# Performance work log

Measured on AMD Instinct MI355X. Metric: run time of the kernel, lower is better.

The kernel has to match this reference:

```python
import jax, jax.numpy as jnp
import numpy as np

VOCAB = 100000
EMB = 256
HID = 512
HH = HID // 2  # per-direction hidden
NTAGS = 12
START = 10
STOP = 11
SEQ = 2048
NEG = -10000.0


def setup_inputs() -> dict:
    key = jax.random.key(0)
    ks = jax.random.split(key, 18)
    s = 0.05
    inp = {
        "sentence": jax.random.randint(ks[0], (SEQ,), 0, VOCAB, dtype=jnp.int64 if jax.config.jax_enable_x64 else jnp.int32),
        "tags": jax.random.randint(ks[1], (SEQ,), 0, 10, dtype=jnp.int64 if jax.config.jax_enable_x64 else jnp.int32),
        "embed": jax.random.normal(ks[2], (VOCAB, EMB), jnp.float32) * s,
        "Wih_f": jax.random.normal(ks[3], (4 * HH, EMB), jnp.float32) * s,
        "Whh_f": jax.random.normal(ks[4], (4 * HH, HH), jnp.float32) * s,
        "bih_f": jax.random.normal(ks[5], (4 * HH,), jnp.float32) * s,
        "bhh_f": jax.random.normal(ks[6], (4 * HH,), jnp.float32) * s,
        "Wih_b": jax.random.normal(ks[7], (4 * HH, EMB), jnp.float32) * s,
        "Whh_b": jax.random.normal(ks[8], (4 * HH, HH), jnp.float32) * s,
        "bih_b": jax.random.normal(ks[9], (4 * HH,), jnp.float32) * s,
        "bhh_b": jax.random.normal(ks[10], (4 * HH,), jnp.float32) * s,
        "W_out": jax.random.normal(ks[11], (NTAGS, HID), jnp.float32) * s,
        "b_out": jax.random.normal(ks[12], (NTAGS,), jnp.float32) * s,
        "h0": jax.random.normal(ks[14], (2, HH), jnp.float32),
        "c0": jax.random.normal(ks[15], (2, HH), jnp.float32),
    }
    trans = jax.random.normal(ks[13], (NTAGS, NTAGS), jnp.float32)
    trans = trans.at[START, :].set(NEG)  # never transition INTO start
    trans = trans.at[:, STOP].set(NEG)   # never transition FROM stop
    inp["transitions"] = trans
    return inp


def _lstm_dir(x, h0, c0, Wih, Whh, bih, bhh):
    # x: [T, E]; PyTorch gate order i, f, g, o
    pre = x @ Wih.T + bih + bhh  # [T, 4*HH] precomputed input projection
    def step(carry, p):
        h, c = carry
        g = p + Whh @ h
        i, f, gg, o = jnp.split(g, 4)
        i = jax.nn.sigmoid(i)
        f = jax.nn.sigmoid(f)
        gg = jnp.tanh(gg)
        o = jax.nn.sigmoid(o)
        c = f * c + i * gg
        h = o * jnp.tanh(c)
        return (h, c), h
    _, hs = jax.lax.scan(step, (h0, c0), pre)
    return hs  # [T, HH]


def _forward_impl(sentence, tags, embed, Wih_f, Whh_f, bih_f, bhh_f,
                  Wih_b, Whh_b, bih_b, bhh_b, W_out, b_out, transitions, h0, c0):
    x = embed[sentence]  # [T, E]
    hf = _lstm_dir(x, h0[0], c0[0], Wih_f, Whh_f, bih_f, bhh_f)
    hb = jnp.flip(_lstm_dir(jnp.flip(x, 0), h0[1], c0[1], Wih_b, Whh_b, bih_b, bhh_b), 0)
    feats = jnp.concatenate([hf, hb], axis=-1) @ W_out.T + b_out  # [T, NTAGS]

    # CRF forward algorithm: log-semiring scan over time
    fv0 = jnp.full((NTAGS,), NEG, feats.dtype).at[START].set(0.0)
    def crf_step(fv, emit):
        # transitions[next, prev]; logsumexp over prev
        fv = jax.nn.logsumexp(fv[None, :] + transitions + emit[:, None], axis=1)
        return fv, None
    fv, _ = jax.lax.scan(crf_step, fv0, feats)
    forward_score = jax.nn.logsumexp(fv + transitions[STOP])

    # gold path score
    prev = jnp.concatenate([jnp.array([START], dtype=tags.dtype), tags[:-1]])
    emit_gold = jnp.take_along_axis(feats, tags[:, None], axis=1)[:, 0]
    gold_score = jnp.sum(transitions[tags, prev]) + jnp.sum(emit_gold) + transitions[STOP, tags[-1]]

    return forward_score - gold_score


def reference(sentence, tags, embed, Wih_f, Whh_f, bih_f, bhh_f,
              Wih_b, Whh_b, bih_b, bhh_b, W_out, b_out, transitions, h0, c0):
    return _forward_impl(sentence, tags, embed, Wih_f, Whh_f, bih_f, bhh_f,
                         Wih_b, Whh_b, bih_b, bhh_b, W_out, b_out, transitions, h0, c0)
```

## Files before the change

kernel.cpp:

```cpp
#include <hip/hip_runtime.h>
#include <hip/hip_bf16.h>
#include <stdint.h>

#define SEQ   2048
#define EMB   256
#define HHD   256
#define GATES 1024
#define NTAGS 12
#define START 10
#define STOP  11
#define CCH   16
#define CLEN  128

__device__ __forceinline__ int sdot4(uint32_t a, uint32_t b, int c) {
#if __has_builtin(__builtin_amdgcn_sdot4)
  return __builtin_amdgcn_sdot4((int)a, (int)b, c, false);
#else
  int r = c;
#pragma unroll
  for (int i = 0; i < 4; i++) {
    int av = (int)(signed char)((a >> (8 * i)) & 255);
    int bv = (int)(signed char)((b >> (8 * i)) & 255);
    r += av * bv;
  }
  return r;
#endif
}

__device__ __forceinline__ float fsig(float x) {
  float e = __expf(-x);
  return __builtin_amdgcn_rcpf(1.0f + e);
}

__global__ __launch_bounds__(256) void k_quant(const float* __restrict__ whh_f,
                                               const float* __restrict__ whh_b,
                                               uint32_t* __restrict__ q4,
                                               float* __restrict__ scales) {
  const int row  = (blockIdx.x * 256 + threadIdx.x) >> 6;
  const int lane = threadIdx.x & 63;
  const int d = row >> 10, r = row & 1023;
  const float4 w = *(const float4*)((d ? whh_b : whh_f) + (long)r * HHD + lane * 4);
  float m = fmaxf(fmaxf(fabsf(w.x), fabsf(w.y)), fmaxf(fabsf(w.z), fabsf(w.w)));
#pragma unroll
  for (int off = 32; off; off >>= 1) m = fmaxf(m, __shfl_xor(m, off, 64));
  m = fmaxf(m, 1e-20f);
  const float inv = 127.f / m;
  int a = (int)rintf(w.x * inv), b = (int)rintf(w.y * inv);
  int c = (int)rintf(w.z * inv), e = (int)rintf(w.w * inv);
  q4[row * 64 + lane] = (uint32_t)(a & 255) | ((uint32_t)(b & 255) << 8) |
                        ((uint32_t)(c & 255) << 16) | ((uint32_t)(e & 255) << 24);
  if (lane == 0) scales[row] = m / 127.f;
}

__global__ __launch_bounds__(256) void k_proj(const int* __restrict__ sentence,
                                              const float* __restrict__ embed,
                                              const float* __restrict__ Wih_f,
                                              const float* __restrict__ bih_f,
                                              const float* __restrict__ bhh_f,
                                              const float* __restrict__ Wih_b,
                                              const float* __restrict__ bih_b,
                                              const float* __restrict__ bhh_b,
                                              float* __restrict__ pre) {
  const int dir = blockIdx.y;
  const int t0  = blockIdx.x * 8;
  const float* Wih = dir ? Wih_b : Wih_f;
  const float* bih = dir ? bih_b : bih_f;
  const float* bhh = dir ? bhh_b : bhh_f;

  __shared__ float xs[8][256];
  const int tid = threadIdx.x;
#pragma unroll
  for (int i = 0; i < 8; i++) {
    int s = sentence[t0 + i];
    xs[i][tid] = embed[(long)s * EMB + tid];
  }
  __syncthreads();

  const int r0 = tid * 4;
  float acc[4][8];
#pragma unroll
  for (int j = 0; j < 4; j++)
#pragma unroll
    for (int t = 0; t < 8; t++) acc[j][t] = 0.f;

  const float4* W4 = (const float4*)Wih;
  for (int kq = 0; kq < 64; kq++) {
    float4 w[4];
#pragma unroll
    for (int j = 0; j < 4; j++) w[j] = W4[(r0 + j) * 64 + kq];
#pragma unroll
    for (int t = 0; t < 8; t++) {
      float4 xv = ((const float4*)xs[t])[kq];
#pragma unroll
      for (int j = 0; j < 4; j++)
        acc[j][t] += w[j].x * xv.x + w[j].y * xv.y + w[j].z * xv.z + w[j].w * xv.w;
    }
  }
#pragma unroll
  for (int j = 0; j < 4; j++) {
    float bsum = bih[r0 + j] + bhh[r0 + j];
#pragma unroll
    for (int t = 0; t < 8; t++)
      pre[((long)(dir * SEQ + t0 + t)) * GATES + r0 + j] = acc[j][t] + bsum;
  }
}

__global__ __launch_bounds__(512, 1) void k_lstm(const uint32_t* __restrict__ q4,
                                                 const float* __restrict__ scales,
                                                 const float* __restrict__ pre,
                                                 const float* __restrict__ h0,
                                                 const float* __restrict__ c0,
                                                 float* __restrict__ hs) {
  const int dir = blockIdx.x;
  const int L   = threadIdx.x;
  const int u   = L >> 1;
  const int odd = L & 1;

  __shared__ __align__(16) uint8_t hbuf[2][256];

  const int rA = (odd ? 512 : 0) + u;
  const int rB = rA + 256;
  const long base = (long)dir * GATES;

  const uint4* qq = (const uint4*)q4;
  uint4 wA[16], wB[16];
#pragma unroll
  for (int j = 0; j < 16; j++) wA[j] = qq[(base + rA) * 16 + j];
#pragma unroll
  for (int j = 0; j < 16; j++) wB[j] = qq[(base + rB) * 16 + j];
  const float sA = scales[base + rA];
  const float sB = scales[base + rB];

  if (L < 256) {
    float v = h0[dir * HHD + L] * (127.f / 4.f);
    v = fminf(fmaxf(v, -127.f), 127.f);
    hbuf[0][L] = (uint8_t)(int)rintf(v);
  }
  float c_st = c0[dir * HHD + u];
  __syncthreads();

  const float* pd = pre + (long)dir * SEQ * GATES;
  float* hsd      = hs  + (long)dir * SEQ * HHD;
  const float gmul = odd ? 2.f : 1.f;

  for (int s = 0; s < SEQ; s++) {
    const int t = dir ? (SEQ - 1 - s) : s;
    const float pre0 = pd[(long)t * GATES + rA];
    const float pre1 = pd[(long)t * GATES + rB];

    const uint4* hq4 = (const uint4*)hbuf[s & 1];
    int a0 = 0, a1 = 0, b0 = 0, b1 = 0;
#pragma unroll
    for (int cc = 0; cc < 16; cc++) {
      uint4 hq = hq4[cc];
      a0 = sdot4(wA[cc].x, hq.x, a0); a1 = sdot4(wA[cc].y, hq.y, a1);
      a0 = sdot4(wA[cc].z, hq.z, a0); a1 = sdot4(wA[cc].w, hq.w, a1);
      b0 = sdot4(wB[cc].x, hq.x, b0); b1 = sdot4(wB[cc].y, hq.y, b1);
      b0 = sdot4(wB[cc].z, hq.z, b0); b1 = sdot4(wB[cc].w, hq.w, b1);
    }
    const float hsc = (s == 0) ? (4.f / 127.f) : (1.f / 127.f);
    const float g0 = pre0 + sA * hsc * (float)(a0 + a1);
    const float g1 = pre1 + sB * hsc * (float)(b0 + b1);

    const float v0 = fsig(g0 * gmul) * gmul - (gmul - 1.f);
    const float v1 = fsig(g1);
    const float p0 = __shfl_xor(v0, 1, 64);
    const float p1 = __shfl_xor(v1, 1, 64);
    const float iv = odd ? p0 : v0;
    const float fv = odd ? p1 : v1;
    const float gv = odd ? v0 : p0;
    const float ov = odd ? v1 : p1;

    c_st = fv * c_st + iv * gv;
    const float hv = ov * (2.f * fsig(2.f * c_st) - 1.f);

    if (!odd) {
      hsd[(long)t * HHD + u] = hv;
    } else {
      hbuf[(s + 1) & 1][u] = (uint8_t)(int)rintf(hv * 127.f);
    }
    __syncthreads();
  }
}

__global__ __launch_bounds__(192) void k_feats(const float* __restrict__ hs,
                                               const float* __restrict__ W_out,
                                               const float* __restrict__ b_out,
                                               float* __restrict__ feats) {
  __shared__ float Wl[12 * 520];
  const int tid = threadIdx.x;
  for (int i = tid; i < 12 * 512; i += 192) Wl[(i / 512) * 520 + (i % 512)] = W_out[i];
  __syncthreads();

  const int tl = tid / 12, n = tid % 12;
  const int t = blockIdx.x * 16 + tl;
  const float4* hf4 = (const float4*)(hs + (long)t * HHD);
  const float4* hb4 = (const float4*)(hs + (long)SEQ * HHD + (long)t * HHD);
  const float4* Wa  = (const float4*)&Wl[n * 520];
  const float4* Wb  = (const float4*)&Wl[n * 520 + 256];

  float acc = b_out[n];
#pragma unroll 8
  for (int j = 0; j < 64; j++) {
    float4 w = Wa[j], h = hf4[j];
    acc += w.x * h.x + w.y * h.y + w.z * h.z + w.w * h.w;
  }
#pragma unroll 8
  for (int j = 0; j < 64; j++) {
    float4 w = Wb[j], h = hb4[j];
    acc += w.x * h.x + w.y * h.y + w.z * h.z + w.w * h.w;
  }
  feats[t * NTAGS + n] = acc;
}

__global__ __launch_bounds__(192) void k_crf_chunk(const float* __restrict__ feats,
                                                   const float* __restrict__ trans,
                                                   float* __restrict__ Pc) {
  const int ch  = blockIdx.x;
  const int tid = threadIdx.x;
  const int n   = tid & 15;
  const int p   = tid >> 4;
  const int nn  = (n < 12) ? n : 11;

  __shared__ float fe[CLEN * NTAGS];
  for (int i = tid; i < CLEN * NTAGS; i += 192) fe[i] = feats[ch * CLEN * NTAGS + i];
  __syncthreads();

  float trn[12];
#pragma unroll
  for (int j = 0; j < 12; j++) trn[j] = trans[nn * 12 + j];

  float Mv = trans[nn * 12 + p] + fe[nn];
  for (int t = 1; t < CLEN; t++) {
    float x[12], m = -1e30f;
#pragma unroll
    for (int j = 0; j < 12; j++) {
      x[j] = trn[j] + __shfl(Mv, (tid & 48) | j, 64);
      m = fmaxf(m, x[j]);
    }
    float ss = 0.f;
#pragma unroll
    for (int j = 0; j < 12; j++) ss += __expf(x[j] - m);
    Mv = fe[t * NTAGS + nn] + m + __logf(ss);
  }
  if (n < 12) Pc[ch * 144 + n * 12 + p] = Mv;
}

__global__ __launch_bounds__(128) void k_crf_final(const float* __restrict__ Pc,
                                                   const float* __restrict__ feats,
                                                   const int* __restrict__ tags,
                                                   const float* __restrict__ trans,
                                                   float* __restrict__ out) {
  __shared__ float Pl[CCH * 144];
  __shared__ float res[2];
  const int tid = threadIdx.x;
  for (int i = tid; i < CCH * 144; i += 128) Pl[i] = Pc[i];
  __syncthreads();

  if (tid < 64) {
    const int n  = tid;
    const int nn = (n < 12) ? n : 11;
    float fv = (n == START) ? 0.f : -10000.f;
    for (int c = 0; c < CCH; c++) {
      float x[12], m = -1e30f;
#pragma unroll
      for (int j = 0; j < 12; j++) {
        x[j] = Pl[c * 144 + nn * 12 + j] + __shfl(fv, j, 64);
        m = fmaxf(m, x[j]);
      }
      float ss = 0.f;
#pragma unroll
      for (int j = 0; j < 12; j++) ss += __expf(x[j] - m);
      fv = m + __logf(ss);
    }
    const float v = fv + trans[STOP * 12 + nn];
    float xs[12], m = -1e30f;
#pragma unroll
    for (int j = 0; j < 12; j++) {
      xs[j] = __shfl(v, j, 64);
      m = fmaxf(m, xs[j]);
    }
    float ss = 0.f;
#pragma unroll
    for (int j = 0; j < 12; j++) ss += __expf(xs[j] - m);
    if (tid == 0) res[0] = m + __logf(ss);
  } else {
    const int i = tid - 64;
    float gp = 0.f;
    for (int b = 0; b < 32; b++) {
      int t  = b * 64 + i;
      int tg = tags[t];
      int pv = (t == 0) ? START : tags[t - 1];
      gp += trans[tg * 12 + pv] + feats[t * NTAGS + tg];
    }
#pragma unroll
    for (int off = 32; off; off >>= 1) gp += __shfl_xor(gp, off, 64);
    if (i == 0) res[1] = gp + trans[STOP * 12 + tags[SEQ - 1]];
  }
  __syncthreads();
  if (tid == 0) out[0] = res[0] - res[1];
}

extern "C" void kernel_launch(void* const* d_in, const int* in_sizes, int n_in,
                              void* d_out, int out_size, void* d_ws, size_t ws_size,
                              hipStream_t stream) {
  const int*   sentence = (const int*)  d_in[0];
  const int*   tags     = (const int*)  d_in[1];
  const float* embed    = (const float*)d_in[2];
  const float* Wih_f    = (const float*)d_in[3];
  const float* Whh_f    = (const float*)d_in[4];
  const float* bih_f    = (const float*)d_in[5];
  const float* bhh_f    = (const float*)d_in[6];
  const float* Wih_b    = (const float*)d_in[7];
  const float* Whh_b    = (const float*)d_in[8];
  const float* bih_b    = (const float*)d_in[9];
  const float* bhh_b    = (const float*)d_in[10];
  const float* W_out    = (const float*)d_in[11];
  const float* b_out    = (const float*)d_in[12];
  const float* h0       = (const float*)d_in[13];
  const float* c0       = (const float*)d_in[14];
  const float* trans    = (const float*)d_in[15];
  float* out = (float*)d_out;

  char* ws = (char*)d_ws;
  uint32_t* q4    = (uint32_t*)ws;
  float*    scales= (float*)(ws + (512l << 10));
  float*    pre   = (float*)(ws + (1l  << 20));
  float*    hs    = (float*)(ws + (17l << 20));
  float*    feats = (float*)(ws + (21l << 20));
  float*    Pc    = (float*)(ws + (21l << 20) + (128l<<10));

  k_quant<<<512, 256, 0, stream>>>(Whh_f, Whh_b, q4, scales);
  k_proj<<<dim3(256, 2), 256, 0, stream>>>(sentence, embed, Wih_f, bih_f, bhh_f,
                                           Wih_b, bih_b, bhh_b, pre);
  k_lstm<<<2, 512, 0, stream>>>(q4, scales, pre, h0, c0, hs);
  k_feats<<<128, 192, 0, stream>>>(hs, W_out, b_out, feats);
  k_crf_chunk<<<CCH, 192, 0, stream>>>(feats, trans, Pc);
  k_crf_final<<<1, 128, 0, stream>>>(Pc, feats, tags, trans, out);
}
```

Baseline: 2.013 ms.

## Split LSTM recurrence dot products across 4 lanes with DPP reductions and interleaved gates

```diff
diff --git a/kernel.cpp b/kernel.cpp
--- a/kernel.cpp
+++ b/kernel.cpp
@@ -30,6 +30,17 @@
 __device__ __forceinline__ float fsig(float x) {
   float e = __expf(-x);
   return __builtin_amdgcn_rcpf(1.0f + e);
+}
+
+__device__ __forceinline__ int dpp_xor1(int x) {
+  return __builtin_amdgcn_update_dpp(0, x, 0xB1, 0xF, 0xF, true);
+}
+__device__ __forceinline__ int dpp_xor2(int x) {
+  return __builtin_amdgcn_update_dpp(0, x, 0x4E, 0xF, 0xF, true);
+}
+__device__ __forceinline__ float dpp_xor2_f(float x) {
+  int r = __builtin_amdgcn_update_dpp(0, __float_as_int(x), 0x4E, 0xF, 0xF, true);
+  return __int_as_float(r);
 }
 
 __global__ __launch_bounds__(256) void k_quant(const float* __restrict__ whh_f,
@@ -98,38 +109,50 @@
   }
 #pragma unroll
   for (int j = 0; j < 4; j++) {
-    float bsum = bih[r0 + j] + bhh[r0 + j];
+    const int row = r0 + j;
+    const int G  = row >> 8;
+    const int uu = row & 255;
+    float bsum = bih[row] + bhh[row];
 #pragma unroll
     for (int t = 0; t < 8; t++)
-      pre[((long)(dir * SEQ + t0 + t)) * GATES + r0 + j] = acc[j][t] + bsum;
-  }
-}
-
-__global__ __launch_bounds__(512, 1) void k_lstm(const uint32_t* __restrict__ q4,
+      pre[(((long)(dir * SEQ + t0 + t)) * HHD + uu) * 4 + G] = acc[j][t] + bsum;
+  }
+}
+
+__global__ __launch_bounds__(512, 2) void k_lstm(const uint32_t* __restrict__ q4,
                                                  const float* __restrict__ scales,
                                                  const float* __restrict__ pre,
                                                  const float* __restrict__ h0,
                                                  const float* __restrict__ c0,
                                                  float* __restrict__ hs) {
-  const int dir = blockIdx.x;
-  const int L   = threadIdx.x;
-  const int u   = L >> 1;
-  const int odd = L & 1;
+  const int dir  = blockIdx.x;
+  const int L    = threadIdx.x;
+  const int q    = L & 3;
+  const int g    = L >> 2;
+  const int p    = q & 1;
+  const int half = q >> 1;
+  const int u    = 2 * g + p;
 
   __shared__ __align__(16) uint8_t hbuf[2][256];
 
-  const int rA = (odd ? 512 : 0) + u;
-  const int rB = rA + 256;
   const long base = (long)dir * GATES;
 
+  uint4 wa[4][4], wb[4][4];
   const uint4* qq = (const uint4*)q4;
-  uint4 wA[16], wB[16];
-#pragma unroll
-  for (int j = 0; j < 16; j++) wA[j] = qq[(base + rA) * 16 + j];
-#pragma unroll
-  for (int j = 0; j < 16; j++) wB[j] = qq[(base + rB) * 16 + j];
-  const float sA = scales[base + rA];
-  const float sB = scales[base + rB];
+#pragma unroll
+  for (int j = 0; j < 4; j++) {
+    const int qj = q ^ j;
+    const int rA = (2 * (qj >> 1)) * 256 + 2 * g + (qj & 1);
+    const int rB = rA + 256;
+#pragma unroll
+    for (int k = 0; k < 4; k++) {
+      wa[j][k] = qq[(base + rA) * 16 + 4 * q + k];
+      wb[j][k] = qq[(base + rB) * 16 + 4 * q + k];
+    }
+  }
+  const int rown = (2 * half) * 256 + u;
+  const float sA = scales[base + rown];
+  const float sB = scales[base + rown + 256];
 
   if (L < 256) {
     float v = h0[dir * HHD + L] * (127.f / 4.f);
@@ -139,46 +162,71 @@
   float c_st = c0[dir * HHD + u];
   __syncthreads();
 
-  const float* pd = pre + (long)dir * SEQ * GATES;
-  float* hsd      = hs  + (long)dir * SEQ * HHD;
-  const float gmul = odd ? 2.f : 1.f;
+  const int t0 = dir ? (SEQ - 1) : 0;
+  const long pstep = dir ? -(long)(HHD * 4) : (long)(HHD * 4);
+  const long hstep = dir ? -(long)HHD : (long)HHD;
+  const float* pp = pre + (long)dir * SEQ * (HHD * 4) + ((long)t0 * HHD + u) * 4 + 2 * half;
+  float* hp       = hs  + (long)dir * SEQ * HHD + (long)t0 * HHD + u;
+  const float gmul = half ? 2.f : 1.f;
+  const int write_h = ((L & 2) == 0);
 
   for (int s = 0; s < SEQ; s++) {
-    const int t = dir ? (SEQ - 1 - s) : s;
-    const float pre0 = pd[(long)t * GATES + rA];
-    const float pre1 = pd[(long)t * GATES + rB];
-
-    const uint4* hq4 = (const uint4*)hbuf[s & 1];
-    int a0 = 0, a1 = 0, b0 = 0, b1 = 0;
-#pragma unroll
-    for (int cc = 0; cc < 16; cc++) {
-      uint4 hq = hq4[cc];
-      a0 = sdot4(wA[cc].x, hq.x, a0); a1 = sdot4(wA[cc].y, hq.y, a1);
-      a0 = sdot4(wA[cc].z, hq.z, a0); a1 = sdot4(wA[cc].w, hq.w, a1);
-      b0 = sdot4(wB[cc].x, hq.x, b0); b1 = sdot4(wB[cc].y, hq.y, b1);
-      b0 = sdot4(wB[cc].z, hq.z, b0); b1 = sdot4(wB[cc].w, hq.w, b1);
-    }
+    const float2 pr = *(const float2*)pp;
+
+    const uint4* hq4 = (const uint4*)(hbuf[s & 1] + (q << 6));
+    const uint4 h0v = hq4[0], h1v = hq4[1], h2v = hq4[2], h3v = hq4[3];
+
+    int pa0 = 0, pa1 = 0, pa2 = 0, pa3 = 0;
+    int pb0 = 0, pb1 = 0, pb2 = 0, pb3 = 0;
+#pragma unroll
+    for (int k = 0; k < 4; k++) {
+      const uint4 hk = (k == 0) ? h0v : (k == 1) ? h1v : (k == 2) ? h2v : h3v;
+      pa0 = sdot4(wa[0][k].x, hk.x, pa0); pa0 = sdot4(wa[0][k].y, hk.y, pa0);
+      pa0 = sdot4(wa[0][k].z, hk.z, pa0); pa0 = sdot4(wa[0][k].w, hk.w, pa0);
+      pa1 = sdot4(wa[1][k].x, hk.x, pa1); pa1 = sdot4(wa[1][k].y, hk.y, pa1);
+      pa1 = sdot4(wa[1][k].z, hk.z, pa1); pa1 = sdot4(wa[1][k].w, hk.w, pa1);
+      pa2 = sdot4(wa[2][k].x, hk.x, pa2); pa2 = sdot4(wa[2][k].y, hk.y, pa2);
+      pa2 = sdot4(wa[2][k].z, hk.z, pa2); pa2 = sdot4(wa[2][k].w, hk.w, pa2);
+      pa3 = sdot4(wa[3][k].x, hk.x, pa3); pa3 = sdot4(wa[3][k].y, hk.y, pa3);
+      pa3 = sdot4(wa[3][k].z, hk.z, pa3); pa3 = sdot4(wa[3][k].w, hk.w, pa3);
+      pb0 = sdot4(wb[0][k].x, hk.x, pb0); pb0 = sdot4(wb[0][k].y, hk.y, pb0);
+      pb0 = sdot4(wb[0][k].z, hk.z, pb0); pb0 = sdot4(wb[0][k].w, hk.w, pb0);
+      pb1 = sdot4(wb[1][k].x, hk.x, pb1); pb1 = sdot4(wb[1][k].y, hk.y, pb1);
+      pb1 = sdot4(wb[1][k].z, hk.z, pb1); pb1 = sdot4(wb[1][k].w, hk.w, pb1);
+      pb2 = sdot4(wb[2][k].x, hk.x, pb2); pb2 = sdot4(wb[2][k].y, hk.y, pb2);
+      pb2 = sdot4(wb[2][k].z, hk.z, pb2); pb2 = sdot4(wb[2][k].w, hk.w, pb2);
+      pb3 = sdot4(wb[3][k].x, hk.x, pb3); pb3 = sdot4(wb[3][k].y, hk.y, pb3);
+      pb3 = sdot4(wb[3][k].z, hk.z, pb3); pb3 = sdot4(wb[3][k].w, hk.w, pb3);
+    }
+    const int tA = pa0 + dpp_xor1(pa1);
+    const int tA2 = pa2 + dpp_xor1(pa3);
+    const int sumA = tA + dpp_xor2(tA2);
+    const int tB = pb0 + dpp_xor1(pb1);
+    const int tB2 = pb2 + dpp_xor1(pb3);
+    const int sumB = tB + dpp_xor2(tB2);
+
     const float hsc = (s == 0) ? (4.f / 127.f) : (1.f / 127.f);
-    const float g0 = pre0 + sA * hsc * (float)(a0 + a1);
-    const float g1 = pre1 + sB * hsc * (float)(b0 + b1);
-
-    const float v0 = fsig(g0 * gmul) * gmul - (gmul - 1.f);
-    const float v1 = fsig(g1);
-    const float p0 = __shfl_xor(v0, 1, 64);
-    const float p1 = __shfl_xor(v1, 1, 64);
-    const float iv = odd ? p0 : v0;
-    const float fv = odd ? p1 : v1;
-    const float gv = odd ? v0 : p0;
-    const float ov = odd ? v1 : p1;
+    const float gA = pr.x + sA * hsc * (float)sumA;
+    const float gB = pr.y + sB * hsc * (float)sumB;
+
+    const float v0 = fsig(gA * gmul) * gmul - (gmul - 1.f);
+    const float v1 = fsig(gB);
+    const float p0 = dpp_xor2_f(v0);
+    const float p1 = dpp_xor2_f(v1);
+    const float iv = half ? p0 : v0;
+    const float fv = half ? p1 : v1;
+    const float gv = half ? v0 : p0;
+    const float ov = half ? v1 : p1;
 
     c_st = fv * c_st + iv * gv;
     const float hv = ov * (2.f * fsig(2.f * c_st) - 1.f);
 
-    if (!odd) {
-      hsd[(long)t * HHD + u] = hv;
-    } else {
+    if (write_h) {
+      *hp = hv;
       hbuf[(s + 1) & 1][u] = (uint8_t)(int)rintf(hv * 127.f);
     }
+    pp += pstep;
+    hp += hstep;
     __syncthreads();
   }
 }
```

After: 1.847 ms. 1.09x faster.

## Split LSTM recurrence between sdot4 and int8 MFMA, fold h0 into preactivations

Applied to the files above, without the earlier changes.

```diff
diff --git a/kernel.cpp b/kernel.cpp
--- a/kernel.cpp
+++ b/kernel.cpp
@@ -1,5 +1,4 @@
 #include <hip/hip_runtime.h>
-#include <hip/hip_bf16.h>
 #include <stdint.h>
 
 #define SEQ   2048
@@ -12,6 +11,10 @@
 #define CCH   16
 #define CLEN  128
 
+typedef int v4i __attribute__((ext_vector_type(4)));
+
+#define LOG2E 1.442695041f
+
 __device__ __forceinline__ int sdot4(uint32_t a, uint32_t b, int c) {
 #if __has_builtin(__builtin_amdgcn_sdot4)
   return __builtin_amdgcn_sdot4((int)a, (int)b, c, false);
@@ -27,19 +30,38 @@
 #endif
 }
 
-__device__ __forceinline__ float fsig(float x) {
-  float e = __expf(-x);
-  return __builtin_amdgcn_rcpf(1.0f + e);
+__device__ __forceinline__ float fexp2(float x) {
+#if __has_builtin(__builtin_amdgcn_exp2f)
+  return __builtin_amdgcn_exp2f(x);
+#else
+  return exp2f(x);
+#endif
+}
+
+__device__ __forceinline__ v4i mfma_i8_16x16x64(v4i a, v4i b, v4i c) {
+#if __has_builtin(__builtin_amdgcn_mfma_i32_16x16x64_i8)
+  return __builtin_amdgcn_mfma_i32_16x16x64_i8(a, b, c, 0, 0, 0);
+#else
+  return c;
+#endif
 }
 
 __global__ __launch_bounds__(256) void k_quant(const float* __restrict__ whh_f,
                                                const float* __restrict__ whh_b,
+                                               const float* __restrict__ h0,
                                                uint32_t* __restrict__ q4,
-                                               float* __restrict__ scales) {
+                                               float* __restrict__ scales,
+                                               float* __restrict__ h0c) {
   const int row  = (blockIdx.x * 256 + threadIdx.x) >> 6;
   const int lane = threadIdx.x & 63;
   const int d = row >> 10, r = row & 1023;
   const float4 w = *(const float4*)((d ? whh_b : whh_f) + (long)r * HHD + lane * 4);
+
+  const float4 hh = *(const float4*)(h0 + d * HHD + lane * 4);
+  float dp = w.x * hh.x + w.y * hh.y + w.z * hh.z + w.w * hh.w;
+#pragma unroll
+  for (int off = 32; off; off >>= 1) dp += __shfl_xor(dp, off, 64);
+
   float m = fmaxf(fmaxf(fabsf(w.x), fabsf(w.y)), fmaxf(fabsf(w.z), fabsf(w.w)));
 #pragma unroll
   for (int off = 32; off; off >>= 1) m = fmaxf(m, __shfl_xor(m, off, 64));
@@ -49,7 +71,7 @@
   int c = (int)rintf(w.z * inv), e = (int)rintf(w.w * inv);
   q4[row * 64 + lane] = (uint32_t)(a & 255) | ((uint32_t)(b & 255) << 8) |
                         ((uint32_t)(c & 255) << 16) | ((uint32_t)(e & 255) << 24);
-  if (lane == 0) scales[row] = m / 127.f;
+  if (lane == 0) { scales[row] = m / 127.f; h0c[row] = dp; }
 }
 
 __global__ __launch_bounds__(256) void k_proj(const int* __restrict__ sentence,
@@ -60,6 +82,7 @@
                                               const float* __restrict__ Wih_b,
                                               const float* __restrict__ bih_b,
                                               const float* __restrict__ bhh_b,
+                                              const float* __restrict__ h0c,
                                               float* __restrict__ pre) {
   const int dir = blockIdx.y;
   const int t0  = blockIdx.x * 8;
@@ -96,90 +119,145 @@
         acc[j][t] += w[j].x * xv.x + w[j].y * xv.y + w[j].z * xv.z + w[j].w * xv.w;
     }
   }
+  const int t0d = dir ? (SEQ - 1) : 0;
 #pragma unroll
   for (int j = 0; j < 4; j++) {
-    float bsum = bih[r0 + j] + bhh[r0 + j];
-#pragma unroll
-    for (int t = 0; t < 8; t++)
-      pre[((long)(dir * SEQ + t0 + t)) * GATES + r0 + j] = acc[j][t] + bsum;
-  }
-}
-
-__global__ __launch_bounds__(512, 1) void k_lstm(const uint32_t* __restrict__ q4,
+    const int row = r0 + j;
+    const int G  = row >> 8;
+    const int uu = row & 255;
+    const float negfac = (G == 2) ? (-2.f * LOG2E) : (-LOG2E);
+    const float bsum = bih[row] + bhh[row];
+    const float c0a  = h0c[dir * GATES + row];
+#pragma unroll
+    for (int t = 0; t < 8; t++) {
+      float v = acc[j][t] + bsum;
+      if (t0 + t == t0d) v += c0a;
+      pre[(((long)(dir * SEQ + t0 + t)) * HHD + uu) * 4 + G] = v * negfac;
+    }
+  }
+}
+
+__global__ __launch_bounds__(512, 2) void k_lstm(const uint32_t* __restrict__ q4,
                                                  const float* __restrict__ scales,
                                                  const float* __restrict__ pre,
-                                                 const float* __restrict__ h0,
                                                  const float* __restrict__ c0,
                                                  float* __restrict__ hs) {
-  const int dir = blockIdx.x;
-  const int L   = threadIdx.x;
-  const int u   = L >> 1;
-  const int odd = L & 1;
+  const int dir  = blockIdx.x;
+  const int L    = threadIdx.x;
+  const int w    = L >> 6;
+  const int lane = L & 63;
+  const long base = (long)dir * GATES;
 
   __shared__ __align__(16) uint8_t hbuf[2][256];
-
-  const int rA = (odd ? 512 : 0) + u;
-  const int rB = rA + 256;
-  const long base = (long)dir * GATES;
-
+  __shared__ __align__(16) int gbufT[4][256];
+
+  const int su   = L >> 2;
+  const int sg   = L & 3;
+  const int srow = sg * 256 + su;
+  uint4 sw[16];
   const uint4* qq = (const uint4*)q4;
-  uint4 wA[16], wB[16];
-#pragma unroll
-  for (int j = 0; j < 16; j++) wA[j] = qq[(base + rA) * 16 + j];
-#pragma unroll
-  for (int j = 0; j < 16; j++) wB[j] = qq[(base + rB) * 16 + j];
-  const float sA = scales[base + rA];
-  const float sB = scales[base + rB];
-
-  if (L < 256) {
-    float v = h0[dir * HHD + L] * (127.f / 4.f);
-    v = fminf(fmaxf(v, -127.f), 127.f);
-    hbuf[0][L] = (uint8_t)(int)rintf(v);
-  }
-  float c_st = c0[dir * HHD + u];
-  __syncthreads();
-
-  const float* pd = pre + (long)dir * SEQ * GATES;
-  float* hsd      = hs  + (long)dir * SEQ * HHD;
-  const float gmul = odd ? 2.f : 1.f;
+#pragma unroll
+  for (int j = 0; j < 16; j++) sw[j] = qq[(base + srow) * 16 + j];
+
+  const int lg  = lane >> 4;
+  const int col = lane & 15;
+  v4i A[4][4];
+#pragma unroll
+  for (int G = 0; G < 4; G++) {
+    const int mrow = G * 256 + 128 + 16 * w + col;
+#pragma unroll
+    for (int kc = 0; kc < 4; kc++) {
+      const uint4 t = qq[(base + mrow) * 16 + kc * 4 + lg];
+      A[G][kc] = (v4i){(int)t.x, (int)t.y, (int)t.z, (int)t.w};
+    }
+  }
+
+  const int  cu      = w * 64 + lane;
+  const bool is_cons = (w < 4);
+  float scv0 = 0.f, scv1 = 0.f, scv2 = 0.f, scv3 = 0.f, c_st = 0.f;
+  const float* pp = nullptr;
+  float* hp = nullptr;
+  long pstep = 0, hstep = 0;
+  if (is_cons) {
+    scv0 = -LOG2E       * scales[base +           cu] * (1.f / 127.f);
+    scv1 = -LOG2E       * scales[base + 256 +     cu] * (1.f / 127.f);
+    scv2 = -2.f * LOG2E * scales[base + 512 +     cu] * (1.f / 127.f);
+    scv3 = -LOG2E       * scales[base + 768 +     cu] * (1.f / 127.f);
+    c_st = c0[dir * HHD + cu];
+    const int t0 = dir ? (SEQ - 1) : 0;
+    pstep = dir ? -(long)(HHD * 4) : (long)(HHD * 4);
+    hstep = dir ? -(long)HHD : (long)HHD;
+    pp = pre + ((long)(dir * SEQ + t0) * HHD + cu) * 4;
+    hp = hs + (long)dir * SEQ * HHD + (long)t0 * HHD + cu;
+  }
+
+  if (L < 256) hbuf[0][L] = 0;
+  __syncthreads();
+
+  float4 pcur = {0.f, 0.f, 0.f, 0.f}, pnext = {0.f, 0.f, 0.f, 0.f};
+  if (is_cons) pcur = *(const float4*)pp;
 
   for (int s = 0; s < SEQ; s++) {
-    const int t = dir ? (SEQ - 1 - s) : s;
-    const float pre0 = pd[(long)t * GATES + rA];
-    const float pre1 = pd[(long)t * GATES + rB];
-
-    const uint4* hq4 = (const uint4*)hbuf[s & 1];
-    int a0 = 0, a1 = 0, b0 = 0, b1 = 0;
-#pragma unroll
-    for (int cc = 0; cc < 16; cc++) {
-      uint4 hq = hq4[cc];
-      a0 = sdot4(wA[cc].x, hq.x, a0); a1 = sdot4(wA[cc].y, hq.y, a1);
-      a0 = sdot4(wA[cc].z, hq.z, a0); a1 = sdot4(wA[cc].w, hq.w, a1);
-      b0 = sdot4(wB[cc].x, hq.x, b0); b1 = sdot4(wB[cc].y, hq.y, b1);
-      b0 = sdot4(wB[cc].z, hq.z, b0); b1 = sdot4(wB[cc].w, hq.w, b1);
-    }
-    const float hsc = (s == 0) ? (4.f / 127.f) : (1.f / 127.f);
-    const float g0 = pre0 + sA * hsc * (float)(a0 + a1);
-    const float g1 = pre1 + sB * hsc * (float)(b0 + b1);
-
-    const float v0 = fsig(g0 * gmul) * gmul - (gmul - 1.f);
-    const float v1 = fsig(g1);
-    const float p0 = __shfl_xor(v0, 1, 64);
-    const float p1 = __shfl_xor(v1, 1, 64);
-    const float iv = odd ? p0 : v0;
-    const float fv = odd ? p1 : v1;
-    const float gv = odd ? v0 : p0;
-    const float ov = odd ? v1 : p1;
-
-    c_st = fv * c_st + iv * gv;
-    const float hv = ov * (2.f * fsig(2.f * c_st) - 1.f);
-
-    if (!odd) {
-      hsd[(long)t * HHD + u] = hv;
-    } else {
-      hbuf[(s + 1) & 1][u] = (uint8_t)(int)rintf(hv * 127.f);
-    }
-    __syncthreads();
+    if (is_cons && s + 1 < SEQ) pnext = *(const float4*)(pp + pstep);
+
+    const uint8_t* hb = hbuf[s & 1];
+    const uint4* h4 = (const uint4*)hb;
+
+    int d0 = 0, d1 = 0, d2 = 0, d3 = 0;
+#pragma unroll
+    for (int j = 0; j < 16; j++) {
+      const uint4 h = h4[j];
+      d0 = sdot4(sw[j].x, h.x, d0);
+      d1 = sdot4(sw[j].y, h.y, d1);
+      d2 = sdot4(sw[j].z, h.z, d2);
+      d3 = sdot4(sw[j].w, h.w, d3);
+    }
+    const int sd = (d0 + d1) + (d2 + d3);
+
+    v4i B[4];
+#pragma unroll
+    for (int kc = 0; kc < 4; kc++) {
+      const uint4 hf = *(const uint4*)(hb + kc * 64 + lg * 16);
+      B[kc] = (v4i){(int)hf.x, (int)hf.y, (int)hf.z, (int)hf.w};
+    }
+    v4i acc[4];
+#pragma unroll
+    for (int G = 0; G < 4; G++) {
+      v4i a = (v4i){0, 0, 0, 0};
+#pragma unroll
+      for (int kc = 0; kc < 4; kc++) a = mfma_i8_16x16x64(A[G][kc], B[kc], a);
+      acc[G] = a;
+    }
+
+    gbufT[sg][su] = sd;
+    if (col == 0) {
+      const int mu = 128 + 16 * w + lg * 4;
+#pragma unroll
+      for (int G = 0; G < 4; G++) *(v4i*)&gbufT[G][mu] = acc[G];
+    }
+    asm volatile("s_waitcnt lgkmcnt(0)\n\ts_barrier" ::: "memory");
+
+    if (is_cons) {
+      const int di = gbufT[0][cu], df = gbufT[1][cu];
+      const int dg = gbufT[2][cu], dq = gbufT[3][cu];
+      const float ai = fmaf(scv0, (float)di, pcur.x);
+      const float af = fmaf(scv1, (float)df, pcur.y);
+      const float ag = fmaf(scv2, (float)dg, pcur.z);
+      const float ao = fmaf(scv3, (float)dq, pcur.w);
+      const float iv = __builtin_amdgcn_rcpf(1.f + fexp2(ai));
+      const float fv = __builtin_amdgcn_rcpf(1.f + fexp2(af));
+      const float gv = fmaf(2.f, __builtin_amdgcn_rcpf(1.f + fexp2(ag)), -1.f);
+      const float ov = __builtin_amdgcn_rcpf(1.f + fexp2(ao));
+      c_st = fmaf(fv, c_st, iv * gv);
+      const float th = fmaf(2.f, __builtin_amdgcn_rcpf(1.f + fexp2(c_st * (-2.f * LOG2E))), -1.f);
+      const float hv = ov * th;
+      *hp = hv;
+      hbuf[(s + 1) & 1][cu] = (uint8_t)(int)rintf(hv * 127.f);
+      pcur = pnext;
+      pp += pstep;
+      hp += hstep;
+    }
+    asm volatile("s_waitcnt lgkmcnt(0)\n\ts_barrier" ::: "memory");
   }
 }
 
@@ -325,15 +403,16 @@
   char* ws = (char*)d_ws;
   uint32_t* q4    = (uint32_t*)ws;
   float*    scales= (float*)(ws + (512l << 10));
+  float*    h0c   = (float*)(ws + (520l << 10));
   float*    pre   = (float*)(ws + (1l  << 20));
   float*    hs    = (float*)(ws + (17l << 20));
   float*    feats = (float*)(ws + (21l << 20));
   float*    Pc    = (float*)(ws + (21l << 20) + (128l<<10));
 
-  k_quant<<<512, 256, 0, stream>>>(Whh_f, Whh_b, q4, scales);
+  k_quant<<<512, 256, 0, stream>>>(Whh_f, Whh_b, h0, q4, scales, h0c);
   k_proj<<<dim3(256, 2), 256, 0, stream>>>(sentence, embed, Wih_f, bih_f, bhh_f,
-                                           Wih_b, bih_b, bhh_b, pre);
-  k_lstm<<<2, 512, 0, stream>>>(q4, scales, pre, h0, c0, hs);
+                                           Wih_b, bih_b, bhh_b, h0c, pre);
+  k_lstm<<<2, 512, 0, stream>>>(q4, scales, pre, c0, hs);
   k_feats<<<128, 192, 0, stream>>>(hs, W_out, b_out, feats);
   k_crf_chunk<<<CCH, 192, 0, stream>>>(feats, trans, Pc);
   k_crf_final<<<1, 128, 0, stream>>>(Pc, feats, tags, trans, out);
```

Result: slower. 2.643 ms (+31.3%).
